# Performance work log

Measured on AMD Instinct MI355X. Metric: run time of the kernel, lower is better.

Reference implementation:

```python
import jax, jax.numpy as jnp
import numpy as np

N_NODES = 100000
N_EDGES = 1600000
HIDDEN = 128
EPS = 0.0


def setup_inputs() -> dict:
    key = jax.random.key(0)
    ks = jax.random.split(key, 9)
    scale = 0.02
    x = jax.random.normal(ks[0], (N_NODES, HIDDEN), dtype=jnp.float32)
    edge_index = jax.random.randint(ks[1], (2, N_EDGES), 0, N_NODES, dtype=jnp.int64)
    edge_weight = jax.random.uniform(ks[2], (N_EDGES,), dtype=jnp.float32)
    # edge_encoder: nn.Linear(1, HIDDEN) -> weight [HIDDEN,1] stored as vector [HIDDEN]
    w_edge = jax.random.normal(ks[3], (HIDDEN,), dtype=jnp.float32) * scale
    b_edge = jnp.zeros((HIDDEN,), dtype=jnp.float32)
    # update_mlp: Linear(H,H) -> ReLU -> Linear(H,H); torch Linear weight is [out,in]
    w1 = jax.random.normal(ks[4], (HIDDEN, HIDDEN), dtype=jnp.float32) * scale
    b1 = jnp.zeros((HIDDEN,), dtype=jnp.float32)
    w2 = jax.random.normal(ks[5], (HIDDEN, HIDDEN), dtype=jnp.float32) * scale
    b2 = jnp.zeros((HIDDEN,), dtype=jnp.float32)
    return {"x": x, "edge_index": edge_index, "edge_weight": edge_weight,
            "w_edge": w_edge, "b_edge": b_edge,
            "w1": w1, "b1": b1, "w2": w2, "b2": b2}


def reference(x, edge_index, edge_weight, w_edge, b_edge, w1, b1, w2, b2):
    src_idx = edge_index[0]
    dst_idx = edge_index[1]
    # edge_encoder(edge_weight[:, None]): [E, H]
    edge_attr = edge_weight[:, None] * w_edge[None, :] + b_edge[None, :]
    # gather src node features + edge bias: [E, H]
    src_features = x[src_idx] + edge_attr
    # scatter-add into per-node buffer: [N, H]
    out = jax.ops.segment_sum(src_features, dst_idx, num_segments=x.shape[0])
    out = out + (1.0 + EPS) * x
    # update_mlp
    out = jax.nn.relu(out @ w1.T + b1) @ w2.T + b2
    return out
```

## Files before the change

kernel.cpp:

```cpp
#include <hip/hip_runtime.h>

#define HID    128
#define LDSW   136
#define NMAX   100000
#define BSH    8
#define BNODES 256
#define NBMAX  ((NMAX + BNODES - 1) / BNODES)
#define CAP    8192
#define EPB    2048
#define BCS    16
#define S8     (5.5f / 127.0f)

typedef __attribute__((ext_vector_type(8))) short bf16x8;
typedef __attribute__((ext_vector_type(4))) short s16x4;
typedef __attribute__((ext_vector_type(4))) float f32x4;

__device__ int           g_bcur[NBMAX * BCS];
__device__ int           g_erec[(size_t)NBMAX * CAP];
__device__ short         g_A[(size_t)NMAX * HID];
__device__ unsigned char g_x8[(size_t)(NMAX + 1) * HID];
__device__ short         g_w1p[HID * HID];
__device__ short         g_w2p[HID * HID];

__device__ __forceinline__ short f2bf(float f) {
    unsigned u = __builtin_bit_cast(unsigned, f);
    unsigned r = (u + 0x7fffu + ((u >> 16) & 1u)) >> 16;
    return (short)r;
}
__device__ __forceinline__ unsigned q8(float f) {
    int t = (int)rintf(f * (127.0f / 5.5f)) + 128;
    t = t < 0 ? 0 : (t > 255 ? 255 : t);
    return (unsigned)t;
}
__device__ __forceinline__ float ub(unsigned u, int k) {
    return (float)((u >> (8 * k)) & 0xFFu);
}

__global__ __launch_bounds__(256) void xcast_kernel(const float* __restrict__ x,
                                                    int n16r, int n16z) {
    int i = blockIdx.x * 256 + threadIdx.x;
    if (i >= n16z) return;
    int4 pk = { 0, 0, 0, 0 };
    if (i < n16r) {
        const float4* p = (const float4*)(x + (size_t)i * 16);
        float4 v0 = p[0], v1 = p[1], v2 = p[2], v3 = p[3];
        pk.x = (int)(q8(v0.x) | (q8(v0.y) << 8) | (q8(v0.z) << 16) | (q8(v0.w) << 24));
        pk.y = (int)(q8(v1.x) | (q8(v1.y) << 8) | (q8(v1.z) << 16) | (q8(v1.w) << 24));
        pk.z = (int)(q8(v2.x) | (q8(v2.y) << 8) | (q8(v2.z) << 16) | (q8(v2.w) << 24));
        pk.w = (int)(q8(v3.x) | (q8(v3.y) << 8) | (q8(v3.z) << 16) | (q8(v3.w) << 24));
    }
    ((int4*)g_x8)[i] = pk;
}

__global__ __launch_bounds__(256) void wpack_kernel(const float* __restrict__ w1,
                                                    const float* __restrict__ w2) {
    int id = blockIdx.x * 256 + threadIdx.x;
    const float* w = (id & 2048) ? w2 : w1;
    short* dst = (id & 2048) ? g_w2p : g_w1p;
    int e = id & 2047;
    int lane = e & 63, kk = (e >> 6) & 3, nt = e >> 8;
    int row = nt * 16 + (lane & 15);
    int col = kk * 32 + (lane >> 4) * 8;
    float4 a = *(const float4*)(w + row * HID + col);
    float4 b = *(const float4*)(w + row * HID + col + 4);
    bf16x8 pk = { f2bf(a.x), f2bf(a.y), f2bf(a.z), f2bf(a.w),
                  f2bf(b.x), f2bf(b.y), f2bf(b.z), f2bf(b.w) };
    *(bf16x8*)(dst + e * 8) = pk;
}

__global__ __launch_bounds__(256) void init_bcur(int nb) {
    int i = blockIdx.x * 256 + threadIdx.x;
    if (i < nb) g_bcur[i * BCS] = i * CAP;
}

__global__ __launch_bounds__(256) void bucket_scatter(
    const int* __restrict__ ei, const float* __restrict__ ew, int nEdges, int nb)
{
    __shared__ int   hist[NBMAX];
    __shared__ int   s_rec[EPB];
    __shared__ short s_b[EPB];
    const int tid = threadIdx.x;
    const int e0 = blockIdx.x * EPB;
    const int cnt = min(EPB, nEdges - e0);

    for (int b = tid; b < nb; b += 256) hist[b] = 0;
    __syncthreads();

    for (int k = tid; k < cnt; k += 256) {
        int e = e0 + k;
        int s = ei[e];
        int d = ei[nEdges + e];
        int bb = d >> BSH;
        int q7 = (int)(ew[e] * 127.0f + 0.5f);
        s_rec[k] = s | ((d & (BNODES - 1)) << 17) | (q7 << 25);
        s_b[k] = (short)bb;
        atomicAdd(&hist[bb], 1);
    }
    __syncthreads();

    for (int b = tid; b < nb; b += 256) {
        int c = hist[b];
        hist[b] = (c > 0) ? atomicAdd(&g_bcur[b * BCS], c) : 0;
    }
    __syncthreads();

    for (int k = tid; k < cnt; k += 256) {
        int rec = s_rec[k];
        int b = s_b[k];
        int slot = atomicAdd(&hist[b], 1);
        g_erec[slot] = rec;
    }
}

__global__ __launch_bounds__(256) void aggregate_kernel(
    const float* __restrict__ w_edge, const float* __restrict__ b_edge, int nNodes)
{
    __shared__ int   s_src[2048];
    __shared__ int   s_off[64 + 1];
    __shared__ int   s_hist[64];
    __shared__ int   s_rank[64];
    __shared__ int   s_sumq[64];

    const int tid = threadIdx.x;
    const int lane = tid & 63;
    const int wave = tid >> 6;
    const int blk = blockIdx.x;
    const int bb = blk >> 2;
    const int qq = blk & 3;
    const int node0 = (bb << BSH) + (qq << 6);
    const int base = bb * CAP;
    const int cnt = g_bcur[bb * BCS] - base;

    if (tid < 64) { s_hist[tid] = 0; s_rank[tid] = 0; s_sumq[tid] = 0; }
    __syncthreads();

    for (int e = tid; e < cnt; e += 256) {
        int rec = g_erec[base + e];
        int loc = (rec >> 17) & 255;
        if ((loc >> 6) == qq) {
            atomicAdd(&s_hist[loc & 63], 1);
            atomicAdd(&s_sumq[loc & 63], (int)((unsigned)rec >> 25));
        }
    }
    __syncthreads();

    if (tid < 64) {
        int v = s_hist[tid];
        int incl = v;
        #pragma unroll
        for (int d = 1; d < 64; d <<= 1) {
            int t = __shfl_up(incl, d, 64);
            if (tid >= d) incl += t;
        }
        s_off[tid] = incl - v;
        if (tid == 63) s_off[64] = incl;
    }
    __syncthreads();

    for (int e = tid; e < cnt; e += 256) {
        int rec = g_erec[base + e];
        int loc = (rec >> 17) & 255;
        if ((loc >> 6) == qq) {
            int r = atomicAdd(&s_rank[loc & 63], 1);
            s_src[s_off[loc & 63] + r] = rec & 0x1FFFF;
        }
    }
    __syncthreads();

    const int g = lane >> 4;
    const int l = lane & 15;
    float4 we0 = ((const float4*)w_edge)[l * 2];
    float4 we1 = ((const float4*)w_edge)[l * 2 + 1];
    float4 be0 = ((const float4*)b_edge)[l * 2];
    float4 be1 = ((const float4*)b_edge)[l * 2 + 1];

    for (int i = 0; i < 16; ++i) {
        int nl = wave * 16 + i;
        int node = node0 + nl;
        int off0 = s_off[nl], off1 = s_off[nl + 1];
        float a0 = 0.f, a1 = 0.f, a2 = 0.f, a3 = 0.f;
        float a4 = 0.f, a5 = 0.f, a6 = 0.f, a7 = 0.f;
        for (int j = off0; j < off1; j += 16) {
            int2 d[4];
            #pragma unroll
            for (int u = 0; u < 4; ++u) {
                int e = j + u * 4 + g;
                int ec = min(e, off1 - 1);
                int s = s_src[ec];
                if (e != ec) s = nNodes;
                d[u] = *(const int2*)(g_x8 + (size_t)s * HID + l * 8);
            }
            #pragma unroll
            for (int u = 0; u < 4; ++u) {
                unsigned ux = (unsigned)d[u].x, uy = (unsigned)d[u].y;
                a0 += ub(ux, 0); a1 += ub(ux, 1); a2 += ub(ux, 2); a3 += ub(ux, 3);
                a4 += ub(uy, 0); a5 += ub(uy, 1); a6 += ub(uy, 2); a7 += ub(uy, 3);
            }
        }
        a0 += __shfl_xor(a0, 16, 64); a1 += __shfl_xor(a1, 16, 64);
        a2 += __shfl_xor(a2, 16, 64); a3 += __shfl_xor(a3, 16, 64);
        a4 += __shfl_xor(a4, 16, 64); a5 += __shfl_xor(a5, 16, 64);
        a6 += __shfl_xor(a6, 16, 64); a7 += __shfl_xor(a7, 16, 64);
        a0 += __shfl_xor(a0, 32, 64); a1 += __shfl_xor(a1, 32, 64);
        a2 += __shfl_xor(a2, 32, 64); a3 += __shfl_xor(a3, 32, 64);
        a4 += __shfl_xor(a4, 32, 64); a5 += __shfl_xor(a5, 32, 64);
        a6 += __shfl_xor(a6, 32, 64); a7 += __shfl_xor(a7, 32, 64);

        if (g == 0 && node < nNodes) {
            int2 ds = *(const int2*)(g_x8 + (size_t)node * HID + l * 8);
            unsigned sx = (unsigned)ds.x, sy = (unsigned)ds.y;
            a0 += ub(sx, 0); a1 += ub(sx, 1); a2 += ub(sx, 2); a3 += ub(sx, 3);
            a4 += ub(sy, 0); a5 += ub(sy, 1); a6 += ub(sy, 2); a7 += ub(sy, 3);
            float dg = (float)(off1 - off0);
            float sw_ = (float)s_sumq[nl] * (1.0f / 127.0f);
            float cc = -128.0f * S8 * (dg + 1.0f);
            float o0 = S8 * a0 + cc + sw_ * we0.x + dg * be0.x;
            float o1 = S8 * a1 + cc + sw_ * we0.y + dg * be0.y;
            float o2 = S8 * a2 + cc + sw_ * we0.z + dg * be0.z;
            float o3 = S8 * a3 + cc + sw_ * we0.w + dg * be0.w;
            float o4 = S8 * a4 + cc + sw_ * we1.x + dg * be1.x;
            float o5 = S8 * a5 + cc + sw_ * we1.y + dg * be1.y;
            float o6 = S8 * a6 + cc + sw_ * we1.z + dg * be1.z;
            float o7 = S8 * a7 + cc + sw_ * we1.w + dg * be1.w;
            int4 pk;
            pk.x = (int)(((unsigned)(unsigned short)f2bf(o0)) | ((unsigned)(unsigned short)f2bf(o1) << 16));
            pk.y = (int)(((unsigned)(unsigned short)f2bf(o2)) | ((unsigned)(unsigned short)f2bf(o3) << 16));
            pk.z = (int)(((unsigned)(unsigned short)f2bf(o4)) | ((unsigned)(unsigned short)f2bf(o5) << 16));
            pk.w = (int)(((unsigned)(unsigned short)f2bf(o6)) | ((unsigned)(unsigned short)f2bf(o7) << 16));
            *(int4*)(g_A + (size_t)node * HID + l * 8) = pk;
        }
    }
}

__global__ __launch_bounds__(256) void mlp_kernel(
    const float* __restrict__ b1, const float* __restrict__ b2,
    float* __restrict__ out, int nNodes, int nTiles)
{
    __shared__ __align__(16) short W1s[HID * HID];
    __shared__ __align__(16) short W2s[HID * HID];
    __shared__ __align__(16) short As[32 * LDSW];

    const int tid = threadIdx.x;
    const int lane = tid & 63;
    const int wave = tid >> 6;
    const int l15 = lane & 15;
    const int quad = lane >> 4;
    const int mrow = (wave & 1) * 16;
    const int ntg0 = (wave >> 1) * 4;

    for (int it = 0; it < 8; ++it) {
        int idx = it * 256 + tid;
        ((int4*)W1s)[idx] = ((const int4*)g_w1p)[idx];
        ((int4*)W2s)[idx] = ((const int4*)g_w2p)[idx];
    }

    float bias1[4], bias2[4];
    #pragma unroll
    for (int nt = 0; nt < 4; ++nt) {
        bias1[nt] = b1[(ntg0 + nt) * 16 + l15];
        bias2[nt] = b2[(ntg0 + nt) * 16 + l15];
    }
    __syncthreads();

    for (int t = blockIdx.x; t < nTiles; t += gridDim.x) {
        int node0 = t * 32;
        for (int it = 0; it < 2; ++it) {
            int idx = it * 256 + tid;
            int r = idx >> 4, c = idx & 15;
            int node = node0 + r;
            int4 v = { 0, 0, 0, 0 };
            if (node < nNodes) v = ((const int4*)(g_A + (size_t)node * HID))[c];
            *(int4*)(As + r * LDSW + c * 8) = v;
        }
        __syncthreads();

        bf16x8 af[4];
        #pragma unroll
        for (int k = 0; k < 4; ++k)
            af[k] = *(const bf16x8*)(As + (mrow + l15) * LDSW + k * 32 + quad * 8);
        f32x4 acc[4];
        #pragma unroll
        for (int nt = 0; nt < 4; ++nt) acc[nt] = (f32x4){0.f, 0.f, 0.f, 0.f};
        #pragma unroll
        for (int nt = 0; nt < 4; ++nt)
            #pragma unroll
            for (int k = 0; k < 4; ++k) {
                bf16x8 bf = *(const bf16x8*)(W1s + (((ntg0 + nt) * 4 + k) * 64 + lane) * 8);
                acc[nt] = __builtin_amdgcn_mfma_f32_16x16x32_bf16(af[k], bf, acc[nt], 0, 0, 0);
            }
        __syncthreads();

        #pragma unroll
        for (int nt = 0; nt < 4; ++nt) {
            int col = (ntg0 + nt) * 16 + l15;
            #pragma unroll
            for (int r = 0; r < 4; ++r) {
                float h = acc[nt][r] + bias1[nt];
                h = h > 0.f ? h : 0.f;
                As[(mrow + quad * 4 + r) * LDSW + col] = f2bf(h);
            }
        }
        __syncthreads();

        #pragma unroll
        for (int k = 0; k < 4; ++k)
            af[k] = *(const bf16x8*)(As + (mrow + l15) * LDSW + k * 32 + quad * 8);
        f32x4 acc2[4];
        #pragma unroll
        for (int nt = 0; nt < 4; ++nt) acc2[nt] = (f32x4){0.f, 0.f, 0.f, 0.f};
        #pragma unroll
        for (int nt = 0; nt < 4; ++nt)
            #pragma unroll
            for (int k = 0; k < 4; ++k) {
                bf16x8 bf = *(const bf16x8*)(W2s + (((ntg0 + nt) * 4 + k) * 64 + lane) * 8);
                acc2[nt] = __builtin_amdgcn_mfma_f32_16x16x32_bf16(af[k], bf, acc2[nt], 0, 0, 0);
            }

        #pragma unroll
        for (int nt = 0; nt < 4; ++nt) {
            int col = (ntg0 + nt) * 16 + l15;
            #pragma unroll
            for (int r = 0; r < 4; ++r) {
                int node = node0 + mrow + quad * 4 + r;
                if (node < nNodes)
                    out[(size_t)node * HID + col] = acc2[nt][r] + bias2[nt];
            }
        }
        __syncthreads();
    }
}

extern "C" void kernel_launch(void* const* d_in, const int* in_sizes, int n_in,
                              void* d_out, int out_size, void* d_ws, size_t ws_size,
                              hipStream_t stream) {
    const float* x      = (const float*)d_in[0];
    const int*   ei     = (const int*)d_in[1];
    const float* ew     = (const float*)d_in[2];
    const float* w_edge = (const float*)d_in[3];
    const float* b_edge = (const float*)d_in[4];
    const float* w1     = (const float*)d_in[5];
    const float* b1     = (const float*)d_in[6];
    const float* w2     = (const float*)d_in[7];
    const float* b2     = (const float*)d_in[8];
    float* out = (float*)d_out;

    int nNodes = in_sizes[0] / HID;
    int nEdges = in_sizes[2];
    int nb = (nNodes + BNODES - 1) >> BSH;
    int nTiles = (nNodes + 31) / 32;

    int n16r = nNodes * (HID / 16);
    int n16z = (nNodes + 1) * (HID / 16);
    xcast_kernel<<<(n16z + 255) / 256, 256, 0, stream>>>(x, n16r, n16z);
    wpack_kernel<<<16, 256, 0, stream>>>(w1, w2);
    init_bcur<<<(nb + 255) / 256, 256, 0, stream>>>(nb);
    bucket_scatter<<<(nEdges + EPB - 1) / EPB, 256, 0, stream>>>(ei, ew, nEdges, nb);
    aggregate_kernel<<<nb * 4, 256, 0, stream>>>(w_edge, b_edge, nNodes);
    mlp_kernel<<<512, 256, 0, stream>>>(b1, b2, out, nNodes, nTiles);
}
```

Before: 245.4 us.

## Stage quarter edges in LDS, pad segments, and accumulate packed uint8 sums

The aggregate kernel now stages this block's quarter of the edge records in shared memory during the first pass, so the second pass over global g_erec is gone. Per-node segments are padded to multiples of 16 with a dummy source index, which removes the clamp-and-mask logic in the inner loop. Each lane now loads 16 bytes per row instead of 8, and accumulates byte pairs in packed 16-bit integer lanes (SWAR) instead of eight float adds per word. The costs are more shared memory, capacity clamps that could silently drop edges if a bucket overflows, and possible 16-bit overflow for very high-degree nodes.

```diff
diff --git a/kernel.cpp b/kernel.cpp
--- a/kernel.cpp
+++ b/kernel.cpp
@@ -9,6 +9,8 @@
 #define CAP    8192
 #define EPB    2048
 #define BCS    16
+#define QCAP   2048
+#define SRCPAD 3072
 #define S8     (5.5f / 127.0f)
 
 typedef __attribute__((ext_vector_type(8))) short bf16x8;
@@ -108,6 +110,7 @@
         int rec = s_rec[k];
         int b = s_b[k];
         int slot = atomicAdd(&hist[b], 1);
+        slot = min(slot, (b + 1) * CAP - 1);
         g_erec[slot] = rec;
     }
 }
@@ -115,11 +118,13 @@
 __global__ __launch_bounds__(256) void aggregate_kernel(
     const float* __restrict__ w_edge, const float* __restrict__ b_edge, int nNodes)
 {
-    __shared__ int   s_src[2048];
-    __shared__ int   s_off[64 + 1];
-    __shared__ int   s_hist[64];
-    __shared__ int   s_rank[64];
-    __shared__ int   s_sumq[64];
+    __shared__ int s_q[QCAP];
+    __shared__ int s_src[SRCPAD];
+    __shared__ int s_poff[64 + 1];
+    __shared__ int s_hist[64];
+    __shared__ int s_rank[64];
+    __shared__ int s_sumq[64];
+    __shared__ int s_qn;
 
     const int tid = threadIdx.x;
     const int lane = tid & 63;
@@ -129,105 +134,121 @@
     const int qq = blk & 3;
     const int node0 = (bb << BSH) + (qq << 6);
     const int base = bb * CAP;
-    const int cnt = g_bcur[bb * BCS] - base;
+    const int cnt = min(g_bcur[bb * BCS] - base, CAP);
 
     if (tid < 64) { s_hist[tid] = 0; s_rank[tid] = 0; s_sumq[tid] = 0; }
+    if (tid == 0) s_qn = 0;
     __syncthreads();
 
     for (int e = tid; e < cnt; e += 256) {
         int rec = g_erec[base + e];
         int loc = (rec >> 17) & 255;
         if ((loc >> 6) == qq) {
-            atomicAdd(&s_hist[loc & 63], 1);
-            atomicAdd(&s_sumq[loc & 63], (int)((unsigned)rec >> 25));
-        }
-    }
-    __syncthreads();
+            int qi = atomicAdd(&s_qn, 1);
+            if (qi < QCAP) {
+                s_q[qi] = rec;
+                atomicAdd(&s_hist[loc & 63], 1);
+                atomicAdd(&s_sumq[loc & 63], (int)((unsigned)rec >> 25));
+            }
+        }
+    }
+    __syncthreads();
+    const int qn = min(s_qn, QCAP);
 
     if (tid < 64) {
         int v = s_hist[tid];
-        int incl = v;
+        int p = (v + 15) & ~15;
+        int pincl = p;
         #pragma unroll
         for (int d = 1; d < 64; d <<= 1) {
-            int t = __shfl_up(incl, d, 64);
-            if (tid >= d) incl += t;
-        }
-        s_off[tid] = incl - v;
-        if (tid == 63) s_off[64] = incl;
-    }
-    __syncthreads();
-
-    for (int e = tid; e < cnt; e += 256) {
-        int rec = g_erec[base + e];
-        int loc = (rec >> 17) & 255;
-        if ((loc >> 6) == qq) {
-            int r = atomicAdd(&s_rank[loc & 63], 1);
-            s_src[s_off[loc & 63] + r] = rec & 0x1FFFF;
-        }
-    }
-    __syncthreads();
-
-    const int g = lane >> 4;
-    const int l = lane & 15;
-    float4 we0 = ((const float4*)w_edge)[l * 2];
-    float4 we1 = ((const float4*)w_edge)[l * 2 + 1];
-    float4 be0 = ((const float4*)b_edge)[l * 2];
-    float4 be1 = ((const float4*)b_edge)[l * 2 + 1];
-
+            int t = __shfl_up(pincl, d, 64);
+            if (tid >= d) pincl += t;
+        }
+        s_poff[tid] = pincl - p;
+        if (tid == 63) s_poff[64] = pincl;
+    }
+    for (int k = tid; k < SRCPAD; k += 256) s_src[k] = nNodes;
+    __syncthreads();
+
+    for (int k = tid; k < qn; k += 256) {
+        int rec = s_q[k];
+        int loc = (rec >> 17) & 63;
+        int r = atomicAdd(&s_rank[loc], 1);
+        int idx = min(s_poff[loc] + r, SRCPAD - 1);
+        s_src[idx] = rec & 0x1FFFF;
+    }
+    __syncthreads();
+
+    const int g = lane >> 3;
+    const int l = lane & 7;
+    float wef[16], bef[16];
+    #pragma unroll
+    for (int c = 0; c < 4; ++c) {
+        float4 tw = ((const float4*)w_edge)[l * 4 + c];
+        float4 tb = ((const float4*)b_edge)[l * 4 + c];
+        wef[c * 4 + 0] = tw.x; wef[c * 4 + 1] = tw.y; wef[c * 4 + 2] = tw.z; wef[c * 4 + 3] = tw.w;
+        bef[c * 4 + 0] = tb.x; bef[c * 4 + 1] = tb.y; bef[c * 4 + 2] = tb.z; bef[c * 4 + 3] = tb.w;
+    }
+
+    const unsigned M = 0x00FF00FFu;
     for (int i = 0; i < 16; ++i) {
         int nl = wave * 16 + i;
         int node = node0 + nl;
-        int off0 = s_off[nl], off1 = s_off[nl + 1];
-        float a0 = 0.f, a1 = 0.f, a2 = 0.f, a3 = 0.f;
-        float a4 = 0.f, a5 = 0.f, a6 = 0.f, a7 = 0.f;
-        for (int j = off0; j < off1; j += 16) {
-            int2 d[4];
-            #pragma unroll
-            for (int u = 0; u < 4; ++u) {
-                int e = j + u * 4 + g;
-                int ec = min(e, off1 - 1);
-                int s = s_src[ec];
-                if (e != ec) s = nNodes;
-                d[u] = *(const int2*)(g_x8 + (size_t)s * HID + l * 8);
-            }
-            #pragma unroll
-            for (int u = 0; u < 4; ++u) {
-                unsigned ux = (unsigned)d[u].x, uy = (unsigned)d[u].y;
-                a0 += ub(ux, 0); a1 += ub(ux, 1); a2 += ub(ux, 2); a3 += ub(ux, 3);
-                a4 += ub(uy, 0); a5 += ub(uy, 1); a6 += ub(uy, 2); a7 += ub(uy, 3);
-            }
-        }
-        a0 += __shfl_xor(a0, 16, 64); a1 += __shfl_xor(a1, 16, 64);
-        a2 += __shfl_xor(a2, 16, 64); a3 += __shfl_xor(a3, 16, 64);
-        a4 += __shfl_xor(a4, 16, 64); a5 += __shfl_xor(a5, 16, 64);
-        a6 += __shfl_xor(a6, 16, 64); a7 += __shfl_xor(a7, 16, 64);
-        a0 += __shfl_xor(a0, 32, 64); a1 += __shfl_xor(a1, 32, 64);
-        a2 += __shfl_xor(a2, 32, 64); a3 += __shfl_xor(a3, 32, 64);
-        a4 += __shfl_xor(a4, 32, 64); a5 += __shfl_xor(a5, 32, 64);
-        a6 += __shfl_xor(a6, 32, 64); a7 += __shfl_xor(a7, 32, 64);
+        int p0 = s_poff[nl], p1 = s_poff[nl + 1];
+        unsigned A[8] = { 0, 0, 0, 0, 0, 0, 0, 0 };
+        for (int j = p0; j < p1; j += 16) {
+            int4 d0 = *(const int4*)(g_x8 + (size_t)s_src[j + g] * HID + l * 16);
+            int4 d1 = *(const int4*)(g_x8 + (size_t)s_src[j + 8 + g] * HID + l * 16);
+            unsigned u;
+            u = (unsigned)d0.x; A[0] += u & M; A[1] += (u >> 8) & M;
+            u = (unsigned)d0.y; A[2] += u & M; A[3] += (u >> 8) & M;
+            u = (unsigned)d0.z; A[4] += u & M; A[5] += (u >> 8) & M;
+            u = (unsigned)d0.w; A[6] += u & M; A[7] += (u >> 8) & M;
+            u = (unsigned)d1.x; A[0] += u & M; A[1] += (u >> 8) & M;
+            u = (unsigned)d1.y; A[2] += u & M; A[3] += (u >> 8) & M;
+            u = (unsigned)d1.z; A[4] += u & M; A[5] += (u >> 8) & M;
+            u = (unsigned)d1.w; A[6] += u & M; A[7] += (u >> 8) & M;
+        }
+        #pragma unroll
+        for (int a = 0; a < 8; ++a) {
+            A[a] += __shfl_xor(A[a], 8, 64);
+            A[a] += __shfl_xor(A[a], 16, 64);
+            A[a] += __shfl_xor(A[a], 32, 64);
+        }
 
         if (g == 0 && node < nNodes) {
-            int2 ds = *(const int2*)(g_x8 + (size_t)node * HID + l * 8);
-            unsigned sx = (unsigned)ds.x, sy = (unsigned)ds.y;
-            a0 += ub(sx, 0); a1 += ub(sx, 1); a2 += ub(sx, 2); a3 += ub(sx, 3);
-            a4 += ub(sy, 0); a5 += ub(sy, 1); a6 += ub(sy, 2); a7 += ub(sy, 3);
-            float dg = (float)(off1 - off0);
+            float fs[16];
+            #pragma unroll
+            for (int d = 0; d < 4; ++d) {
+                fs[d * 4 + 0] = (float)(A[2 * d] & 0xFFFFu);
+                fs[d * 4 + 2] = (float)(A[2 * d] >> 16);
+                fs[d * 4 + 1] = (float)(A[2 * d + 1] & 0xFFFFu);
+                fs[d * 4 + 3] = (float)(A[2 * d + 1] >> 16);
+            }
+            int4 ds = *(const int4*)(g_x8 + (size_t)node * HID + l * 16);
+            unsigned sd[4] = { (unsigned)ds.x, (unsigned)ds.y, (unsigned)ds.z, (unsigned)ds.w };
+            #pragma unroll
+            for (int d = 0; d < 4; ++d) {
+                fs[d * 4 + 0] += ub(sd[d], 0);
+                fs[d * 4 + 1] += ub(sd[d], 1);
+                fs[d * 4 + 2] += ub(sd[d], 2);
+                fs[d * 4 + 3] += ub(sd[d], 3);
+            }
+            float dg = (float)s_hist[nl];
             float sw_ = (float)s_sumq[nl] * (1.0f / 127.0f);
             float cc = -128.0f * S8 * (dg + 1.0f);
-            float o0 = S8 * a0 + cc + sw_ * we0.x + dg * be0.x;
-            float o1 = S8 * a1 + cc + sw_ * we0.y + dg * be0.y;
-            float o2 = S8 * a2 + cc + sw_ * we0.z + dg * be0.z;
-            float o3 = S8 * a3 + cc + sw_ * we0.w + dg * be0.w;
-            float o4 = S8 * a4 + cc + sw_ * we1.x + dg * be1.x;
-            float o5 = S8 * a5 + cc + sw_ * we1.y + dg * be1.y;
-            float o6 = S8 * a6 + cc + sw_ * we1.z + dg * be1.z;
-            float o7 = S8 * a7 + cc + sw_ * we1.w + dg * be1.w;
-            int4 pk;
-            pk.x = (int)(((unsigned)(unsigned short)f2bf(o0)) | ((unsigned)(unsigned short)f2bf(o1) << 16));
-            pk.y = (int)(((unsigned)(unsigned short)f2bf(o2)) | ((unsigned)(unsigned short)f2bf(o3) << 16));
-            pk.z = (int)(((unsigned)(unsigned short)f2bf(o4)) | ((unsigned)(unsigned short)f2bf(o5) << 16));
-            pk.w = (int)(((unsigned)(unsigned short)f2bf(o6)) | ((unsigned)(unsigned short)f2bf(o7) << 16));
-            *(int4*)(g_A + (size_t)node * HID + l * 8) = pk;
+            unsigned pk[8];
+            #pragma unroll
+            for (int d = 0; d < 8; ++d) {
+                float oa = S8 * fs[2 * d] + cc + sw_ * wef[2 * d] + dg * bef[2 * d];
+                float ob = S8 * fs[2 * d + 1] + cc + sw_ * wef[2 * d + 1] + dg * bef[2 * d + 1];
+                pk[d] = ((unsigned)(unsigned short)f2bf(oa)) |
+                        ((unsigned)(unsigned short)f2bf(ob) << 16);
+            }
+            int4 o0 = { (int)pk[0], (int)pk[1], (int)pk[2], (int)pk[3] };
+            int4 o1 = { (int)pk[4], (int)pk[5], (int)pk[6], (int)pk[7] };
+            *(int4*)(g_A + (size_t)node * HID + l * 16) = o0;
+            *(int4*)(g_A + (size_t)node * HID + l * 16 + 8) = o1;
         }
     }
 }
```

After: 247.5 us. Within noise of the previous version (+0.9%).
